# Performance work log

Hardware: AMD Instinct MI355X
Metric: run time of the kernel (lower is better)

## Reference

```python
import jax, jax.numpy as jnp
import numpy as np

DIM = 512
L = 4096
B, H, W = 8, 64, 64
EPS = 1e-06
BN_EPS = 1e-05


def setup_inputs() -> dict:
    key = jax.random.key(0)
    ks = jax.random.split(key, 16)
    s = 1.0 / np.sqrt(DIM)
    d = {
        'x': jax.random.normal(ks[0], (B, DIM, H, W), dtype=jnp.float32),
        'pos_emb': jax.random.normal(ks[1], (1, L, DIM), dtype=jnp.float32),
        'Wq': jax.random.uniform(ks[2], (DIM, DIM), jnp.float32, -s, s),
        'bq': jax.random.uniform(ks[3], (DIM,), jnp.float32, -s, s),
        'Wk': jax.random.uniform(ks[4], (DIM, DIM), jnp.float32, -s, s),
        'bk': jax.random.uniform(ks[5], (DIM,), jnp.float32, -s, s),
        'Wv': jax.random.uniform(ks[6], (DIM, DIM), jnp.float32, -s, s),
        'bv': jax.random.uniform(ks[7], (DIM,), jnp.float32, -s, s),
        'Wq1': jax.random.uniform(ks[8], (DIM, DIM), jnp.float32, -s, s),
        'bq1': jax.random.uniform(ks[9], (DIM,), jnp.float32, -s, s),
        'Wk1': jax.random.uniform(ks[10], (DIM, DIM), jnp.float32, -s, s),
        'bk1': jax.random.uniform(ks[11], (DIM,), jnp.float32, -s, s),
        'gamma': jax.random.normal(ks[12], (1,), jnp.float32) * 0.1,
        'bn_weight': jnp.ones((DIM,), jnp.float32),
        'bn_bias': jnp.zeros((DIM,), jnp.float32),
    }
    return d


def reference(x, pos_emb, Wq, bq, Wk, bk, Wv, bv, Wq1, bq1, Wk1, bk1, gamma, bn_weight, bn_bias):
    Bb, C, Hh, Ww = x.shape
    # [B,C,H,W] -> [B, L, C] tokens
    xs = x.transpose(0, 2, 3, 1).reshape(Bb, Hh * Ww, C) + pos_emb
    Q = jax.nn.relu(xs @ Wq.T + bq)   # kernel_fun = ReLU
    K = jax.nn.relu(xs @ Wk.T + bk)
    V = xs @ Wv.T + bv
    Q1 = xs @ Wq1.T + bq1
    K1 = xs @ Wk1.T + bk1
    # torch einsum 'blc,bcc,bl->blc' uses only diag(KV); compute it directly:
    # diagKV[b,c] = sum_l K[b,l,c] * V[b,l,c]
    diagKV = jnp.einsum('blc,blc->bc', K, V)
    Ksum = K.sum(axis=1)  # == K^T summed over last axis, [B,C]
    Z = 1.0 / jnp.einsum('blc,bc->bl', Q, Ksum + EPS)
    result = Q * diagKV[:, None, :] * Z[:, :, None]  # [B,L,C]
    # channel-softmax attention: softmax over last dim of Q1^T @ K1, [B,C,C]
    mid = jax.nn.softmax(jnp.einsum('blc,bld->bcd', Q1, K1), axis=-1)
    result = result @ mid  # [B,L,C]
    xs = xs + gamma * result
    y = xs.transpose(0, 2, 1).reshape(Bb, C, Hh, Ww)
    # BatchNorm2d in training mode (fresh module): batch stats, biased variance
    mean = y.mean(axis=(0, 2, 3))
    var = y.var(axis=(0, 2, 3))
    yn = (y - mean[None, :, None, None]) * jax.lax.rsqrt(var + BN_EPS)[None, :, None, None]
    yn = yn * bn_weight[None, :, None, None] + bn_bias[None, :, None, None]
    return jax.nn.relu(yn)
```

## Files before the change

kernel.cpp:

```cpp
#include <hip/hip_runtime.h>
#include <stdint.h>

typedef float f32x4 __attribute__((ext_vector_type(4)));
typedef short bf16x8 __attribute__((ext_vector_type(8)));

__device__ __forceinline__ float bf2f(unsigned short h){
  union { unsigned int u; float f; } v; v.u = ((unsigned int)h) << 16; return v.f;
}
__device__ __forceinline__ unsigned short f2bf(float f){
  union { float f; unsigned int u; } v; v.f = f;
  return (unsigned short)((v.u + 0x7fffu + ((v.u >> 16) & 1u)) >> 16);
}

typedef __attribute__((address_space(1))) const unsigned int ga_u32;
typedef __attribute__((address_space(3))) unsigned int ls_u32;
__device__ __forceinline__ void async_load16(const void* g, void* l){
  __builtin_amdgcn_global_load_lds((ga_u32*)g, (ls_u32*)l, 16, 0, 0);
}

#define CFENCE() asm volatile("" ::: "memory")
#define SB0() __builtin_amdgcn_sched_barrier(0)

__global__ __launch_bounds__(256) void k_prep_w(
    const float* __restrict__ w0, const float* __restrict__ w1,
    const float* __restrict__ w2, const float* __restrict__ w3,
    const float* __restrict__ w4, unsigned short* __restrict__ out)
{
  int i = blockIdx.x * 256 + threadIdx.x;
  const float* w = (blockIdx.y == 0) ? w0 : (blockIdx.y == 1) ? w1 :
                   (blockIdx.y == 2) ? w2 : (blockIdx.y == 3) ? w3 : w4;
  out[(size_t)blockIdx.y * 262144 + i] = f2bf(w[i]);
}
__global__ __launch_bounds__(256) void k_prep_b(
    const float* __restrict__ b0, const float* __restrict__ b1,
    const float* __restrict__ b2, const float* __restrict__ b3,
    const float* __restrict__ b4, float* __restrict__ out)
{
  int i = blockIdx.x * 256 + threadIdx.x;
  int s = i >> 9, r = i & 511;
  const float* b = (s == 0) ? b0 : (s == 1) ? b1 : (s == 2) ? b2 : (s == 3) ? b3 : b4;
  out[i] = b[r];
}
__global__ __launch_bounds__(256) void k_prep_dup(
    const unsigned short* __restrict__ wbf, unsigned short* __restrict__ wq1x2)
{
  const int e = blockIdx.x;
  const int t = threadIdx.x;
  #pragma unroll
  for (int rep = 0; rep < 2; rep++){
    int idx = rep*256 + t;
    unsigned short v = wbf[3*262144 + e*512 + idx];
    wq1x2[(size_t)e*1024 + idx] = v;
    wq1x2[(size_t)e*1024 + 512 + idx] = v;
  }
}

__global__ __launch_bounds__(256) void k_build_xs(
    const float* __restrict__ x, const float* __restrict__ pos,
    unsigned short* __restrict__ xsb, unsigned short* __restrict__ xsT,
    float* __restrict__ svec)
{
  __shared__ float tile[64][65];
  __shared__ unsigned short tile2[64][72];
  __shared__ float sred[256];
  const int lt = blockIdx.x, ct = blockIdx.y;
  const int t = threadIdx.x;
  const int rr = t >> 3, c8 = (t & 7) * 8;
  float pr[16];
  #pragma unroll
  for (int pass = 0; pass < 2; pass++){
    int gl = lt*64 + rr + pass*32;
    f32x4 p0 = *(const f32x4*)(pos + (size_t)gl * 512 + ct*64 + c8);
    f32x4 p1 = *(const f32x4*)(pos + (size_t)gl * 512 + ct*64 + c8 + 4);
    #pragma unroll
    for (int s = 0; s < 4; s++){ pr[pass*8+s] = p0[s]; pr[pass*8+4+s] = p1[s]; }
  }
  for (int b = 0; b < 8; b++){
    #pragma unroll
    for (int pass = 0; pass < 2; pass++){
      int r = rr + pass * 32;
      const float* src = x + ((size_t)b * 512 + ct*64 + r) * 4096 + lt*64 + c8;
      f32x4 v0 = *(const f32x4*)src;
      f32x4 v1 = *(const f32x4*)(src + 4);
      #pragma unroll
      for (int s = 0; s < 4; s++){ tile[r][c8+s] = v0[s]; tile[r][c8+4+s] = v1[s]; }
    }
    __syncthreads();
    #pragma unroll
    for (int pass = 0; pass < 2; pass++){
      int ll = rr + pass * 32;
      int gl = lt*64 + ll;
      bf16x8 hv;
      #pragma unroll
      for (int s = 0; s < 8; s++){
        unsigned short h = f2bf(tile[c8+s][ll] + pr[pass*8+s]);
        hv[s] = (short)h;
        tile2[c8+s][ll] = h;
      }
      *(bf16x8*)(xsb + ((size_t)b * 4096 + gl) * 512 + ct*64 + c8) = hv;
    }
    __syncthreads();
    #pragma unroll
    for (int rep = 0; rep < 2; rep++){
      int c = rep*32 + (t >> 3);
      int l0 = (t & 7) * 8;
      bf16x8 v = *(const bf16x8*)&tile2[c][l0];
      *(bf16x8*)(xsT + ((size_t)b * 512 + ct*64 + c) * 4096 + lt*64 + l0) = v;
    }
    {
      const int c = t & 63, lq = t >> 6;
      float s_ = 0.f;
      #pragma unroll
      for (int j = 0; j < 16; j++) s_ += bf2f(tile2[c][lq*16 + j]);
      sred[t] = s_;
      __syncthreads();
      if (t < 64){
        float ss = sred[t] + sred[t+64] + sred[t+128] + sred[t+192];
        atomicAdd(&svec[b*512 + ct*64 + t], ss);
      }
    }
    __syncthreads();
  }
}

__global__ __launch_bounds__(256) void k_uw(
    const unsigned short* __restrict__ wbf, const float* __restrict__ svec,
    float* __restrict__ u, float* __restrict__ w)
{
  __shared__ float sv[512];
  const int sel = blockIdx.x, b = blockIdx.y;
  const int t = threadIdx.x;
  sv[t] = svec[b*512 + t]; sv[t+256] = svec[b*512 + t + 256];
  __syncthreads();
  const unsigned short* Wp = wbf + (size_t)(3 + sel) * 262144;
  float* o = sel ? w : u;
  #pragma unroll
  for (int rep = 0; rep < 2; rep++){
    int e = rep*256 + t;
    const unsigned short* row = Wp + (size_t)e * 512;
    float acc = 0.f;
    for (int ch = 0; ch < 64; ch++){
      bf16x8 v = *(const bf16x8*)(row + ch*8);
      #pragma unroll
      for (int j = 0; j < 8; j++) acc += bf2f((unsigned short)v[j]) * sv[ch*8+j];
    }
    o[b*512 + e] = acc;
  }
}

__global__ __launch_bounds__(256) void k_z(
    const unsigned short* __restrict__ Qb, const float* __restrict__ ksum,
    float* __restrict__ Z)
{
  const int row = blockIdx.x * 4 + (threadIdx.x >> 6);
  const int lane = threadIdx.x & 63;
  const int b = row >> 12;
  bf16x8 q = *(const bf16x8*)(Qb + (size_t)row * 512 + lane * 8);
  f32x4 k0 = *(const f32x4*)(ksum + b*512 + lane*8);
  f32x4 k1 = *(const f32x4*)(ksum + b*512 + lane*8 + 4);
  float den = 0.f;
  #pragma unroll
  for (int s = 0; s < 4; s++) den += bf2f((unsigned short)q[s])   * (k0[s] + 1e-6f);
  #pragma unroll
  for (int s = 0; s < 4; s++) den += bf2f((unsigned short)q[4+s]) * (k1[s] + 1e-6f);
  #pragma unroll
  for (int m = 1; m < 64; m <<= 1) den += __shfl_xor(den, m);
  if (lane == 0) Z[row] = 1.0f / den;
}

__global__ __launch_bounds__(64) void k_softmax(
    const float* __restrict__ S, unsigned short* __restrict__ mid)
{
  const size_t row = blockIdx.x;
  const int lane = threadIdx.x;
  const float* p = S + row * 512 + lane * 8;
  f32x4 v0 = *(const f32x4*)p, v1 = *(const f32x4*)(p + 4);
  float mx = v0[0];
  #pragma unroll
  for (int s = 1; s < 4; s++) mx = fmaxf(mx, v0[s]);
  #pragma unroll
  for (int s = 0; s < 4; s++) mx = fmaxf(mx, v1[s]);
  #pragma unroll
  for (int m = 1; m < 64; m <<= 1) mx = fmaxf(mx, __shfl_xor(mx, m));
  float e[8]; float sum = 0.f;
  #pragma unroll
  for (int s = 0; s < 4; s++){ e[s]   = __expf(v0[s] - mx); sum += e[s]; }
  #pragma unroll
  for (int s = 0; s < 4; s++){ e[4+s] = __expf(v1[s] - mx); sum += e[4+s]; }
  #pragma unroll
  for (int m = 1; m < 64; m <<= 1) sum += __shfl_xor(sum, m);
  float inv = 1.0f / sum;
  bf16x8 hv;
  #pragma unroll
  for (int s = 0; s < 8; s++) hv[s] = (short)f2bf(e[s] * inv);
  *(bf16x8*)(mid + row * 512 + lane * 8) = hv;
}

__global__ __launch_bounds__(256) void k_transpose_scale(
    const unsigned short* __restrict__ in, const float* __restrict__ diag,
    unsigned short* __restrict__ out)
{
  __shared__ float tile[64][65];
  const int rt = blockIdx.x, ct = blockIdx.y, z = blockIdx.z;
  const unsigned short* src = in  + (size_t)z * 262144;
  unsigned short*       dst = out + (size_t)z * 262144;
  const int t = threadIdx.x;
  const int rr = t >> 3, c8 = (t & 7) * 8;
  #pragma unroll
  for (int pass = 0; pass < 2; pass++){
    int r = rr + pass * 32;
    bf16x8 v = *(const bf16x8*)(src + (size_t)(rt*64 + r) * 512 + ct*64 + c8);
    #pragma unroll
    for (int s = 0; s < 8; s++) tile[r][c8+s] = bf2f((unsigned short)v[s]);
  }
  __syncthreads();
  f32x4 dg0 = *(const f32x4*)(diag + z*512 + rt*64 + c8);
  f32x4 dg1 = *(const f32x4*)(diag + z*512 + rt*64 + c8 + 4);
  #pragma unroll
  for (int pass = 0; pass < 2; pass++){
    int c = rr + pass * 32;
    bf16x8 hv;
    #pragma unroll
    for (int s = 0; s < 4; s++) hv[s]   = (short)f2bf(tile[c8+s][c]   * dg0[s]);
    #pragma unroll
    for (int s = 0; s < 4; s++) hv[4+s] = (short)f2bf(tile[c8+4+s][c] * dg1[s]);
    *(bf16x8*)(dst + (size_t)(ct*64 + c) * 512 + rt*64 + c8) = hv;
  }
}

#define GEMM_PRE()                                                            \
  const int tid = threadIdx.x;                                                \
  const int lane = tid & 63;                                                  \
  const int wave = tid >> 6;                                                  \
  const int wm = wave >> 1, wn = wave & 1;                                    \
  size_t aoff[4], boff[4]; int ldsq[4];                                       \
  _Pragma("unroll")                                                           \
  for (int i = 0; i < 4; i++){                                                \
    int qq = i*4 + wave;                                                      \
    int ch = qq*64 + lane;                                                    \
    int m  = ch >> 3, p = ch & 7;                                             \
    int lc = p ^ (m & 7);                                                     \
    aoff[i] = (size_t)(m0 + m) * K + lc*8;                                    \
    boff[i] = (size_t)m * K + lc*8;                                           \
    ldsq[i] = qq * 1024;                                                      \
  }                                                                           \
  f32x4 acc[4][4];                                                            \
  const f32x4 vzero = {0.f,0.f,0.f,0.f};                                      \
  _Pragma("unroll")                                                           \
  for (int i = 0; i < 4; i++)                                                 \
    _Pragma("unroll")                                                         \
    for (int j = 0; j < 4; j++) acc[i][j] = vzero;                            \
  int arow[4], brow[4];                                                       \
  _Pragma("unroll")                                                           \
  for (int f = 0; f < 4; f++){                                                \
    arow[f] = (wm*64 + f*16 + (lane & 15)) * 64;                              \
    brow[f] = (wn*64 + f*16 + (lane & 15)) * 64;                              \
  }                                                                           \
  const int kg = lane >> 4;                                                   \
  const int l7 = lane & 7;                                                    \
  const int l15 = lane & 15;

#define GEMM_STAGE2(buf, kt, BB)                                              \
  _Pragma("unroll")                                                           \
  for (int i = 0; i < 4; i++){                                                \
    async_load16(Ae + aoff[i] + (kt)*64, (char*)&smem[(buf)*8192] + ldsq[i]); \
    async_load16((BB) + boff[i] + (kt)*64, (char*)&smem[16384 + (buf)*8192] + ldsq[i]); \
  }

#define GEMM_COMPUTE2(buf, ACC)                                               \
  _Pragma("unroll")                                                           \
  for (int ks = 0; ks < 2; ks++){                                             \
    bf16x8 a[4], b[4];                                                        \
    const int pa = (ks*4 + kg) ^ l7;                                          \
    _Pragma("unroll")                                                         \
    for (int f = 0; f < 4; f++){                                              \
      a[f] = *(const bf16x8*)&smem[(buf)*8192 + arow[f] + pa*8];              \
      b[f] = *(const bf16x8*)&smem[16384 + (buf)*8192 + brow[f] + pa*8];      \
    }                                                                         \
    _Pragma("unroll")                                                         \
    for (int i = 0; i < 4; i++)                                               \
      _Pragma("unroll")                                                       \
      for (int j = 0; j < 4; j++)                                             \
        (ACC)[i][j] = __builtin_amdgcn_mfma_f32_16x16x32_bf16(a[i], b[j], (ACC)[i][j], 0, 0, 0); \
  }

#define GEMM_KLOOP2(nkt, BB)                                                  \
  GEMM_STAGE2(0, 0, BB);                                                      \
  __syncthreads();                                                            \
  { int cur = 0;                                                              \
    for (int kt = 0; kt < (nkt); kt++){                                       \
      if (kt + 1 < (nkt)) { GEMM_STAGE2(cur ^ 1, kt + 1, BB); }               \
      GEMM_COMPUTE2(cur, acc);                                                \
      __syncthreads();                                                        \
      cur ^= 1;                                                               \
    } }

__global__ __launch_bounds__(256) void gemm_G(
    const unsigned short* __restrict__ A,
    unsigned short* __restrict__ Gstk)
{
  __shared__ unsigned short smem[32768];
  const int bid = blockIdx.x;
  const int wgid = (bid & 7) * 32 + (bid >> 3);
  const int part = wgid & 1;
  const int ntile = (wgid >> 1) & 3;
  const int mtile = (wgid >> 3) & 3;
  const int z = wgid >> 5;
  const int m0 = mtile * 128, n0 = ntile * 128;
  const int K = 4096;
  const unsigned short* Ae = A + (size_t)z * 2097152 + part * 2048;
  const unsigned short* Be = Ae + (size_t)n0 * 4096;

  GEMM_PRE();
  GEMM_KLOOP2(32, Be);

  #pragma unroll
  for (int j = 0; j < 4; j++){
    const int cl = wn*64 + j*16 + l15;
    #pragma unroll
    for (int i = 0; i < 4; i++){
      const int rb = wm*64 + i*16 + kg*4;
      #pragma unroll
      for (int q = 0; q < 4; q++)
        smem[(rb + q)*136 + cl] = f2bf(acc[i][j][q]);
    }
  }
  __syncthreads();
  #pragma unroll
  for (int rep = 0; rep < 8; rep++){
    const int rl = rep*16 + (tid >> 4);
    const int c0 = (tid & 15) * 8;
    bf16x8 v = *(const bf16x8*)&smem[rl*136 + c0];
    *(bf16x8*)(Gstk + (size_t)z*524288 + (size_t)(m0 + rl)*1024 + part*512 + n0 + c0) = v;
  }
}

__global__ __launch_bounds__(256) void gemm_P(
    const unsigned short* __restrict__ Wq1x2,
    const unsigned short* __restrict__ Gstk,
    unsigned short* __restrict__ P)
{
  __shared__ unsigned short smem[32768];
  const int bid = blockIdx.x;
  const int wgid = (bid & 7) * 16 + (bid >> 3);
  const int z = wgid >> 4;
  const int mtile = (wgid >> 2) & 3, ntile = wgid & 3;
  const int m0 = mtile * 128, n0 = ntile * 128;
  const int K = 1024;
  const unsigned short* Ae = Wq1x2;
  const unsigned short* Be = Gstk + (size_t)z * 524288 + (size_t)n0 * 1024;

  GEMM_PRE();
  GEMM_KLOOP2(16, Be);

  #pragma unroll
  for (int j = 0; j < 4; j++){
    const int cl = wn*64 + j*16 + l15;
    #pragma unroll
    for (int i = 0; i < 4; i++){
      const int rb = wm*64 + i*16 + kg*4;
      #pragma unroll
      for (int q = 0; q < 4; q++)
        smem[(rb + q)*136 + cl] = f2bf(acc[i][j][q]);
    }
  }
  __syncthreads();
  #pragma unroll
  for (int rep = 0; rep < 8; rep++){
    const int rl = rep*16 + (tid >> 4);
    const int c0 = (tid & 15) * 8;
    bf16x8 v = *(const bf16x8*)&smem[rl*136 + c0];
    *(bf16x8*)(P + (size_t)z * 262144 + (size_t)(m0 + rl) * 512 + n0 + c0) = v;
  }
}

__global__ __launch_bounds__(256) void gemm_S(
    const unsigned short* __restrict__ P,
    const unsigned short* __restrict__ Wk1b,
    const float* __restrict__ bias5,
    const float* __restrict__ u, const float* __restrict__ w,
    float* __restrict__ Sf)
{
  __shared__ unsigned short smem[32768];
  const int bid = blockIdx.x;
  const int wgid = (bid & 7) * 16 + (bid >> 3);
  const int z = wgid >> 4;
  const int mtile = (wgid >> 2) & 3, ntile = wgid & 3;
  const int m0 = mtile * 128, n0 = ntile * 128;
  const int K = 512;
  const unsigned short* Ae = P + (size_t)z * 262144;
  const unsigned short* Be = Wk1b + (size_t)n0 * 512;

  GEMM_PRE();
  GEMM_KLOOP2(8, Be);

  #pragma unroll
  for (int j = 0; j < 4; j++){
    int cd = n0 + wn*64 + j*16 + l15;
    float bkv = bias5[2048 + cd];
    float wv  = w[z*512 + cd] + 4096.0f * bkv;
    #pragma unroll
    for (int i = 0; i < 4; i++){
      int r = m0 + wm*64 + i*16 + kg*4;
      #pragma unroll
      for (int q = 0; q < 4; q++){
        int rr = r + q;
        float uq  = u[z*512 + rr];
        float bqv = bias5[1536 + rr];
        Sf[(size_t)z * 262144 + (size_t)rr * 512 + cd] =
            acc[i][j][q] + uq * bkv + bqv * wv;
      }
    }
  }
}

__global__ __launch_bounds__(256, 2) void gemm_proj2(
    const unsigned short* __restrict__ A,
    const unsigned short* __restrict__ W,
    const float* __restrict__ bias5,
    unsigned short* __restrict__ Qb,
    float* __restrict__ diag, float* __restrict__ ksum)
{
  __shared__ unsigned short smem[32768];
  const int bid = blockIdx.x;
  const int wgid = (bid & 7) * 256 + (bid >> 3);
  const int mtile = wgid >> 3;
  const int unit  = wgid & 7;
  const int m0 = mtile * 128;
  const int K = 512;
  const unsigned short* Ae = A;

  int mode, cb;
  const unsigned short* BeK; const unsigned short* BeV = W;
  if (unit < 4){ mode = 0; cb = unit*128;     BeK = W + (size_t)cb * 512; }
  else         { mode = 1; cb = (unit-4)*128; BeK = W + 262144 + (size_t)cb * 512;
                                              BeV = W + 524288 + (size_t)cb * 512; }

  GEMM_PRE();

  if (mode == 1){
    const int bz = mtile >> 5;
    GEMM_STAGE2(0, 0, BeK);
    __syncthreads();
    int cur = 0;
    for (int kt = 0; kt < 8; kt++){
      if (kt < 7) { GEMM_STAGE2(cur ^ 1, kt + 1, BeK); }
      else        { GEMM_STAGE2(cur ^ 1, 0, BeV); }
      GEMM_COMPUTE2(cur, acc);
      __syncthreads();
      cur ^= 1;
    }
    GEMM_STAGE2(cur ^ 1, 1, BeV);
    unsigned int kpk[4][4][2];
    #pragma unroll
    for (int j = 0; j < 4; j++){
      const int cj = cb + wn*64 + j*16 + l15;
      const float bb = bias5[512 + cj];
      float ks_ = 0.f;
      #pragma unroll
      for (int i = 0; i < 4; i++){
        #pragma unroll
        for (int h = 0; h < 2; h++){
          float v0 = acc[i][j][2*h]   + bb; v0 = v0 > 0.f ? v0 : 0.f;
          float v1 = acc[i][j][2*h+1] + bb; v1 = v1 > 0.f ? v1 : 0.f;
          unsigned short h0 = f2bf(v0), h1 = f2bf(v1);
          kpk[i][j][h] = (unsigned)h0 | ((unsigned)h1 << 16);
          ks_ += bf2f(h0) + bf2f(h1);
        }
        acc[i][j] = vzero;
      }
      ks_ += __shfl_xor(ks_, 16);
      ks_ += __shfl_xor(ks_, 32);
      if (lane < 16) atomicAdd(&ksum[bz*512 + cj], ks_);
    }
    for (int kt = 0; kt < 8; kt++){
      if (kt >= 1 && kt < 7) { GEMM_STAGE2(cur ^ 1, kt + 1, BeV); }
      GEMM_COMPUTE2(cur, acc);
      __syncthreads();
      cur ^= 1;
    }
    #pragma unroll
    for (int j = 0; j < 4; j++){
      const int cj = cb + wn*64 + j*16 + l15;
      const float bb = bias5[1024 + cj];
      float dv = 0.f;
      #pragma unroll
      for (int i = 0; i < 4; i++){
        #pragma unroll
        for (int h = 0; h < 2; h++){
          float v0 = bf2f(f2bf(acc[i][j][2*h]   + bb));
          float v1 = bf2f(f2bf(acc[i][j][2*h+1] + bb));
          dv += bf2f((unsigned short)(kpk[i][j][h] & 0xffffu)) * v0
              + bf2f((unsigned short)(kpk[i][j][h] >> 16))     * v1;
        }
      }
      dv += __shfl_xor(dv, 16);
      dv += __shfl_xor(dv, 32);
      if (lane < 16) atomicAdd(&diag[bz*512 + cj], dv);
    }
    return;
  }

  GEMM_KLOOP2(8, BeK);

  #pragma unroll
  for (int j = 0; j < 4; j++){
    const int cl = wn*64 + j*16 + l15;
    const float bb = bias5[cb + cl];
    #pragma unroll
    for (int i = 0; i < 4; i++){
      const int rb = wm*64 + i*16 + kg*4;
      #pragma unroll
      for (int q = 0; q < 4; q++){
        float v = acc[i][j][q] + bb; v = v > 0.f ? v : 0.f;
        smem[(rb + q)*136 + cl] = f2bf(v);
      }
    }
  }
  __syncthreads();
  #pragma unroll
  for (int rep = 0; rep < 8; rep++){
    const int rl = rep*16 + (tid >> 4);
    const int c0 = (tid & 15) * 8;
    bf16x8 v = *(const bf16x8*)&smem[rl*136 + c0];
    *(bf16x8*)(Qb + (size_t)(m0 + rl) * 512 + cb + c0) = v;
  }
}

#define G8_PRE(AE)                                                            \
  const int t = threadIdx.x;                                                  \
  const int lane = t & 63;                                                    \
  const int wave = t >> 6;                                                    \
  const int wm = wave >> 2, wn = wave & 3;                                    \
  const int l15 = lane & 15, kg = lane >> 4;                                  \
  const int lcw = ((t & 7) ^ ((t >> 3) & 7)) * 8;                             \
  const unsigned short* a_src = (AE) + (size_t)(m0 + (t >> 3)) * 512 + lcw;   \
  f32x4 acc[8][4];                                                            \
  const f32x4 vzero = {0.f,0.f,0.f,0.f};                                      \
  _Pragma("unroll")                                                           \
  for (int i = 0; i < 8; i++)                                                 \
    _Pragma("unroll")                                                         \
    for (int j = 0; j < 4; j++) acc[i][j] = vzero;                            \
  bf16x8 af[4][2], bf[4][2];

#define STAGE_A(D,H,TT) do{                                                   \
  async_load16(a_src + (H)*65536 + (TT)*64,                                   \
               (char*)smem + ((D)*16384 + (H)*8192 + t*8)*2);                 \
  async_load16(a_src + (H)*65536 + 32768 + (TT)*64,                           \
               (char*)smem + ((D)*16384 + (H)*8192 + 4096 + t*8)*2);          \
}while(0)

#define STAGE_B(D,H,TT) do{                                                   \
  async_load16(b_src + (H)*65536 + (TT)*64,                                   \
               (char*)smem + (32768 + (D)*16384 + (H)*8192 + t*8)*2);         \
  async_load16(b_src + (H)*65536 + 32768 + (TT)*64,                           \
               (char*)smem + (32768 + (D)*16384 + (H)*8192 + 4096 + t*8)*2);  \
}while(0)

#define READ_A(D, MH) do{                                                     \
  _Pragma("unroll")                                                           \
  for (int mfl = 0; mfl < 4; ++mfl){                                          \
    const int rl = ((MH)*4 + mfl)*16 + l15;                                   \
    _Pragma("unroll")                                                         \
    for (int ks = 0; ks < 2; ++ks){                                           \
      const int ck = (ks*4 + kg) ^ (rl & 7);                                  \
      af[mfl][ks] = *(const bf16x8*)&smem[(D)*16384 + wm*8192 + rl*64 + ck*8];\
    }                                                                         \
  }                                                                           \
}while(0)

#define READ_B(D, NP) do{                                                     \
  _Pragma("unroll")                                                           \
  for (int nfl = 0; nfl < 2; ++nfl){                                          \
    const int nf = (NP)*2 + nfl;                                              \
    const int rbl = (wn & 1)*64 + nf*16 + l15;                                \
    _Pragma("unroll")                                                         \
    for (int ks = 0; ks < 2; ++ks){                                           \
      const int ck = (ks*4 + kg) ^ (rbl & 7);                                 \
      bf[nf][ks] = *(const bf16x8*)&smem[32768 + (D)*16384 + (wn>>1)*8192 + rbl*64 + ck*8]; \
    }                                                                         \
  }                                                                           \
}while(0)

#define QUAD(MH, NP)                                                          \
  _Pragma("unroll")                                                           \
  for (int mfl = 0; mfl < 4; ++mfl)                                           \
    _Pragma("unroll")                                                         \
    for (int nfl = 0; nfl < 2; ++nfl)                                         \
      _Pragma("unroll")                                                       \
      for (int ks = 0; ks < 2; ++ks)                                          \
        acc[(MH)*4+mfl][(NP)*2+nfl] = __builtin_amdgcn_mfma_f32_16x16x32_bf16(\
            af[mfl][ks], bf[(NP)*2+nfl][ks], acc[(MH)*4+mfl][(NP)*2+nfl], 0,0,0);

#define PH_MID()  CFENCE(); __builtin_amdgcn_s_barrier();                     \
  __builtin_amdgcn_s_setprio(1); SB0()
#define PH_END()  SB0(); __builtin_amdgcn_s_setprio(0); CFENCE();             \
  __builtin_amdgcn_s_barrier(); CFENCE()
#define PH_END_VM4() SB0(); __builtin_amdgcn_s_setprio(0);                    \
  asm volatile("s_waitcnt vmcnt(4)" ::: "memory");                            \
  __builtin_amdgcn_s_barrier(); CFENCE()
#define PH_END_VM0() SB0(); __builtin_amdgcn_s_setprio(0);                    \
  asm volatile("s_waitcnt vmcnt(0)" ::: "memory");                            \
  __builtin_amdgcn_s_barrier(); CFENCE()

#define G8_KLOOP()                                                            \
  STAGE_A(0,0,0); STAGE_A(0,1,0); STAGE_B(0,0,0); STAGE_B(0,1,0);             \
  STAGE_B(1,0,1); STAGE_B(1,1,1);                                             \
  asm volatile("s_waitcnt vmcnt(4)" ::: "memory");                            \
  __builtin_amdgcn_s_barrier(); CFENCE();                                     \
  for (int it = 0; it < 3; ++it){                                             \
    const int t1 = 2*it + 1, t2 = 2*it + 2, t3 = 2*it + 3;                    \
    READ_A(0,0); READ_B(0,0); STAGE_A(1,0,t1);                                \
    PH_MID(); QUAD(0,0); PH_END();                                            \
    READ_B(0,1); STAGE_A(1,1,t1);                                             \
    PH_MID(); QUAD(0,1); PH_END();                                            \
    READ_A(0,1); STAGE_B(0,0,t2);                                             \
    PH_MID(); QUAD(1,0); PH_END();                                            \
    STAGE_A(0,0,t2);                                                          \
    PH_MID(); QUAD(1,1); PH_END_VM4();                                        \
    READ_A(1,0); READ_B(1,0); STAGE_A(0,1,t2);                                \
    PH_MID(); QUAD(0,0); PH_END();                                            \
    READ_B(1,1); STAGE_B(0,1,t2);                                             \
    PH_MID(); QUAD(0,1); PH_END();                                            \
    READ_A(1,1); STAGE_B(1,0,t3);                                             \
    PH_MID(); QUAD(1,0); PH_END();                                            \
    STAGE_B(1,1,t3);                                                          \
    PH_MID(); QUAD(1,1); PH_END_VM4();                                        \
  }                                                                           \
  { READ_A(0,0); READ_B(0,0); STAGE_A(1,0,7);                                 \
    PH_MID(); QUAD(0,0); PH_END();                                            \
    READ_B(0,1); STAGE_A(1,1,7);                                              \
    PH_MID(); QUAD(0,1); PH_END();                                            \
    READ_A(0,1);                                                              \
    PH_MID(); QUAD(1,0); PH_END();                                            \
    PH_MID(); QUAD(1,1); PH_END_VM0();                                        \
    READ_A(1,0); READ_B(1,0);                                                 \
    PH_MID(); QUAD(0,0); PH_END();                                            \
    READ_B(1,1);                                                              \
    PH_MID(); QUAD(0,1); PH_END();                                            \
    READ_A(1,1);                                                              \
    PH_MID(); QUAD(1,0); PH_END();                                            \
    PH_MID(); QUAD(1,1); PH_END(); }

__global__ __launch_bounds__(512, 2) void gemm8_res(
    const unsigned short* __restrict__ A,
    const unsigned short* __restrict__ Bt,
    const float* __restrict__ Zp,
    unsigned short* __restrict__ outh,
    const float* __restrict__ gamma_p,
    float* __restrict__ bnS, float* __restrict__ bnQ)
{
  __shared__ unsigned short smem[65536];
  __shared__ float zbuf[256];
  const int bid = blockIdx.x;
  const int wgid = (bid & 7) * 32 + (bid >> 3);
  const int mtile = wgid >> 1;
  const int ntile = wgid & 1;
  const int m0 = mtile * 256;
  const int nc0 = ntile * 256;

  G8_PRE(A);
  const unsigned short* b_src =
      Bt + (size_t)(mtile >> 4) * 262144 + (size_t)(nc0 + (t >> 3)) * 512 + lcw;

  G8_KLOOP();

  const float g = gamma_p[0];
  __syncthreads();
  if (t < 256) zbuf[t] = Zp[m0 + t];
  __syncthreads();
  #pragma unroll
  for (int nf = 0; nf < 4; nf++){
    int cl = wn*64 + nf*16 + l15;
    #pragma unroll
    for (int mf = 0; mf < 8; mf++){
      int rbase = wm*128 + mf*16 + kg*4;
      #pragma unroll
      for (int q = 0; q < 4; q++){
        int rl = rbase + q;
        smem[rl*256 + (cl ^ (((rl >> 2) & 3) << 4))] =
            f2bf(g * zbuf[rl] * acc[mf][nf][q]);
      }
    }
  }
  __syncthreads();
  float sc[8] = {0.f,0.f,0.f,0.f,0.f,0.f,0.f,0.f};
  float sq[8] = {0.f,0.f,0.f,0.f,0.f,0.f,0.f,0.f};
  const int c0 = (t & 31) * 8;
  #pragma unroll
  for (int rep = 0; rep < 16; rep++){
    int rl = rep*16 + (t >> 5);
    bf16x8 ga = *(const bf16x8*)&smem[rl*256 + (c0 ^ (((rl >> 2) & 3) << 4))];
    size_t gidx = (size_t)(m0 + rl) * 512 + nc0 + c0;
    bf16x8 xv = *(const bf16x8*)(outh + gidx);
    bf16x8 yv;
    #pragma unroll
    for (int j = 0; j < 8; j++){
      float y = bf2f((unsigned short)xv[j]) + bf2f((unsigned short)ga[j]);
      yv[j] = (short)f2bf(y);
      sc[j] += y; sq[j] += y * y;
    }
    *(bf16x8*)(outh + gidx) = yv;
  }
  __syncthreads();
  float* red = (float*)(void*)smem;
  const int tg = t >> 5;
  f32x4 s0 = {sc[0],sc[1],sc[2],sc[3]}, s1 = {sc[4],sc[5],sc[6],sc[7]};
  f32x4 q0 = {sq[0],sq[1],sq[2],sq[3]}, q1 = {sq[4],sq[5],sq[6],sq[7]};
  *(f32x4*)&red[tg*256 + c0]        = s0;  *(f32x4*)&red[tg*256 + c0 + 4]        = s1;
  *(f32x4*)&red[4096 + tg*256 + c0] = q0;  *(f32x4*)&red[4096 + tg*256 + c0 + 4] = q1;
  __syncthreads();
  if (t < 256){
    float ss = 0.f, qq = 0.f;
    #pragma unroll
    for (int gg = 0; gg < 16; gg++){
      ss += red[gg*256 + t];
      qq += red[4096 + gg*256 + t];
    }
    atomicAdd(&bnS[nc0 + t], ss);
    atomicAdd(&bnQ[nc0 + t], qq);
  }
}

__global__ __launch_bounds__(256) void k_bn_finalize(
    const unsigned short* __restrict__ y, const float* __restrict__ bnS,
    const float* __restrict__ bnQ, const float* __restrict__ bnw,
    const float* __restrict__ bnb, float* __restrict__ out)
{
  __shared__ float tile[64][65];
  __shared__ float scale_s[64], shift_s[64];
  const int lt = blockIdx.x, ct = blockIdx.y, b = blockIdx.z;
  const int t = threadIdx.x;
  if (t < 64){
    int c = ct*64 + t;
    float s = bnS[c], q = bnQ[c];
    float mean = s * (1.0f / 32768.0f);
    float var  = q * (1.0f / 32768.0f) - mean * mean;
    float inv  = rsqrtf(var + 1e-5f);
    float scv  = bnw[c] * inv;
    scale_s[t] = scv;
    shift_s[t] = bnb[c] - mean * scv;
  }
  const int rr = t >> 3, c8 = (t & 7) * 8;
  #pragma unroll
  for (int pass = 0; pass < 2; pass++){
    int l = rr + pass * 32;
    bf16x8 v = *(const bf16x8*)(y + ((size_t)b * 4096 + lt*64 + l) * 512 + ct*64 + c8);
    #pragma unroll
    for (int s = 0; s < 8; s++) tile[l][c8+s] = bf2f((unsigned short)v[s]);
  }
  __syncthreads();
  #pragma unroll
  for (int pass = 0; pass < 2; pass++){
    int c = rr + pass * 32;
    float scv = scale_s[c], sh = shift_s[c];
    f32x4 o0, o1;
    #pragma unroll
    for (int s = 0; s < 4; s++){
      float v = tile[c8+s][c] * scv + sh;     o0[s] = v > 0.f ? v : 0.f;
      float w = tile[c8+4+s][c] * scv + sh;   o1[s] = w > 0.f ? w : 0.f;
    }
    float* dp = out + ((size_t)b * 512 + ct*64 + c) * 4096 + lt*64 + c8;
    *(f32x4*)dp = o0;
    *(f32x4*)(dp + 4) = o1;
  }
}

extern "C" void kernel_launch(void* const* d_in, const int* in_sizes, int n_in,
                              void* d_out, int out_size, void* d_ws, size_t ws_size,
                              hipStream_t stream)
{
  const float* x    = (const float*)d_in[0];
  const float* pos  = (const float*)d_in[1];
  const float* Wq   = (const float*)d_in[2];
  const float* bq   = (const float*)d_in[3];
  const float* Wk   = (const float*)d_in[4];
  const float* bk   = (const float*)d_in[5];
  const float* Wv   = (const float*)d_in[6];
  const float* bv   = (const float*)d_in[7];
  const float* Wq1  = (const float*)d_in[8];
  const float* bq1  = (const float*)d_in[9];
  const float* Wk1  = (const float*)d_in[10];
  const float* bk1  = (const float*)d_in[11];
  const float* gam  = (const float*)d_in[12];
  const float* bnw  = (const float*)d_in[13];
  const float* bnb  = (const float*)d_in[14];
  float* out = (float*)d_out;
  char* ws = (char*)d_ws;

  const size_t MB = 1ull << 20;
  const size_t OFF_XSB  = 0;
  const size_t OFF_QB   = 32*MB;
  const size_t OFF_XST  = 64*MB;
  const size_t OFF_GSTK = 96*MB;
  const size_t OFF_PBF  = 104*MB;
  const size_t OFF_SF   = 108*MB;
  const size_t OFF_MIDB = 116*MB;
  const size_t OFF_MIDT = 120*MB;
  const size_t OFF_WBF  = 124*MB;
  const size_t OFF_WQ2  = 127*MB;
  const size_t OFF_B5   = 128*MB + 512*1024;
  const size_t OFF_UV   = 129*MB;
  const size_t OFF_WV   = OFF_UV + 16384;
  const size_t OFF_Z    = OFF_WV + 16384;
  const size_t OFF_DIAG = 130*MB;
  const size_t OFF_KSUM = OFF_DIAG + 16384;
  const size_t OFF_BNS  = OFF_KSUM + 16384;
  const size_t OFF_BNQ  = OFF_BNS + 2048;
  const size_t OFF_SV   = OFF_BNQ + 2048;
  const size_t ZERO_LEN = 16384 + 16384 + 2048 + 2048 + 16384;
  const size_t WS_NEED  = OFF_SV + 16384;
  if (ws_size < WS_NEED) return;

  unsigned short* xsb  = (unsigned short*)(ws + OFF_XSB);
  unsigned short* Qb   = (unsigned short*)(ws + OFF_QB);
  unsigned short* xsT  = (unsigned short*)(ws + OFF_XST);
  unsigned short* Gstk = (unsigned short*)(ws + OFF_GSTK);
  unsigned short* Pbf  = (unsigned short*)(ws + OFF_PBF);
  float*          Sf   = (float*)(ws + OFF_SF);
  unsigned short* midb = (unsigned short*)(ws + OFF_MIDB);
  unsigned short* midT = (unsigned short*)(ws + OFF_MIDT);
  unsigned short* wbf  = (unsigned short*)(ws + OFF_WBF);
  unsigned short* wq1x2= (unsigned short*)(ws + OFF_WQ2);
  float* bias5 = (float*)(ws + OFF_B5);
  float* uvec = (float*)(ws + OFF_UV);
  float* wvec = (float*)(ws + OFF_WV);
  float* Zp   = (float*)(ws + OFF_Z);
  float* diag = (float*)(ws + OFF_DIAG);
  float* ksum = (float*)(ws + OFF_KSUM);
  float* bnS  = (float*)(ws + OFF_BNS);
  float* bnQ  = (float*)(ws + OFF_BNQ);
  float* svec = (float*)(ws + OFF_SV);

  hipMemsetAsync(ws + OFF_DIAG, 0, ZERO_LEN, stream);

  k_prep_w  <<<dim3(1024, 5), 256, 0, stream>>>(Wq, Wk, Wv, Wq1, Wk1, wbf);
  k_prep_b  <<<dim3(10),      256, 0, stream>>>(bq, bk, bv, bq1, bk1, bias5);
  k_prep_dup<<<dim3(512),     256, 0, stream>>>(wbf, wq1x2);

  k_build_xs<<<dim3(64, 8), 256, 0, stream>>>(x, pos, xsb, xsT, svec);

  gemm_proj2<<<dim3(2048), 256, 0, stream>>>(xsb, wbf, bias5, Qb, diag, ksum);

  k_uw<<<dim3(2, 8), 256, 0, stream>>>(wbf, svec, uvec, wvec);

  gemm_G<<<dim3(256), 256, 0, stream>>>(xsT, Gstk);

  gemm_P<<<dim3(128), 256, 0, stream>>>(wq1x2, Gstk, Pbf);
  gemm_S<<<dim3(128), 256, 0, stream>>>(Pbf, wbf + 4*262144, bias5, uvec, wvec, Sf);

  k_z<<<dim3(8192), 256, 0, stream>>>(Qb, ksum, Zp);

  k_softmax<<<dim3(4096), 64, 0, stream>>>(Sf, midb);
  k_transpose_scale<<<dim3(8, 8, 8), 256, 0, stream>>>(midb, diag, midT);

  gemm8_res<<<dim3(256), 512, 0, stream>>>(Qb, midT, Zp, xsb, gam, bnS, bnQ);

  k_bn_finalize<<<dim3(64, 8, 8), 256, 0, stream>>>(xsb, bnS, bnQ, bnw, bnb, out);
}
```

Measured before the change: 246.1 us.

## Merge prep kernels and co-schedule Gram, projection and u/w work in one launch

The three weight/bias prep kernels are folded into a single launch, and the Wq1 duplicate is now converted straight from fp32 so it no longer depends on the earlier bf16 copy. The Gram GEMM (gemm_G), the projection GEMM (gemm_proj2) and the small u/w matvec (k_uw) are combined into one mega-kernel that dispatches on block index, with the long K=4096 Gram tiles placed first. The aim is to cut launch gaps and let the long Gram blocks overlap with the many short projection tiles instead of running serially. In exchange the Gram path is now limited by the launch_bounds(256,2) occupancy hint of the merged kernel, and k_z is moved ahead of gemm_P/S.

```diff
diff --git a/kernel.cpp b/kernel.cpp
--- a/kernel.cpp
+++ b/kernel.cpp
@@ -21,37 +21,39 @@
 #define CFENCE() asm volatile("" ::: "memory")
 #define SB0() __builtin_amdgcn_sched_barrier(0)
 
-__global__ __launch_bounds__(256) void k_prep_w(
+__global__ __launch_bounds__(256) void k_prep_all(
     const float* __restrict__ w0, const float* __restrict__ w1,
     const float* __restrict__ w2, const float* __restrict__ w3,
-    const float* __restrict__ w4, unsigned short* __restrict__ out)
-{
-  int i = blockIdx.x * 256 + threadIdx.x;
-  const float* w = (blockIdx.y == 0) ? w0 : (blockIdx.y == 1) ? w1 :
-                   (blockIdx.y == 2) ? w2 : (blockIdx.y == 3) ? w3 : w4;
-  out[(size_t)blockIdx.y * 262144 + i] = f2bf(w[i]);
-}
-__global__ __launch_bounds__(256) void k_prep_b(
+    const float* __restrict__ w4,
     const float* __restrict__ b0, const float* __restrict__ b1,
     const float* __restrict__ b2, const float* __restrict__ b3,
-    const float* __restrict__ b4, float* __restrict__ out)
-{
-  int i = blockIdx.x * 256 + threadIdx.x;
-  int s = i >> 9, r = i & 511;
-  const float* b = (s == 0) ? b0 : (s == 1) ? b1 : (s == 2) ? b2 : (s == 3) ? b3 : b4;
-  out[i] = b[r];
-}
-__global__ __launch_bounds__(256) void k_prep_dup(
-    const unsigned short* __restrict__ wbf, unsigned short* __restrict__ wq1x2)
-{
-  const int e = blockIdx.x;
+    const float* __restrict__ b4,
+    unsigned short* __restrict__ wbf, float* __restrict__ bias5,
+    unsigned short* __restrict__ wq1x2)
+{
+  const int bid = blockIdx.x;
   const int t = threadIdx.x;
-  #pragma unroll
-  for (int rep = 0; rep < 2; rep++){
-    int idx = rep*256 + t;
-    unsigned short v = wbf[3*262144 + e*512 + idx];
-    wq1x2[(size_t)e*1024 + idx] = v;
-    wq1x2[(size_t)e*1024 + 512 + idx] = v;
+  if (bid < 5120){
+    int slot = bid >> 10;
+    int i = (bid & 1023) * 256 + t;
+    const float* w = (slot == 0) ? w0 : (slot == 1) ? w1 :
+                     (slot == 2) ? w2 : (slot == 3) ? w3 : w4;
+    wbf[(size_t)slot * 262144 + i] = f2bf(w[i]);
+  } else if (bid < 5130){
+    int i = (bid - 5120) * 256 + t;
+    int s = i >> 9, r = i & 511;
+    const float* b = (s == 0) ? b0 : (s == 1) ? b1 : (s == 2) ? b2 :
+                     (s == 3) ? b3 : b4;
+    bias5[i] = b[r];
+  } else {
+    int e = bid - 5130;
+    #pragma unroll
+    for (int rep = 0; rep < 2; rep++){
+      int idx = rep*256 + t;
+      unsigned short v = f2bf(w3[e*512 + idx]);
+      wq1x2[(size_t)e*1024 + idx] = v;
+      wq1x2[(size_t)e*1024 + 512 + idx] = v;
+    }
   }
 }
 
@@ -120,31 +122,6 @@
       }
     }
     __syncthreads();
-  }
-}
-
-__global__ __launch_bounds__(256) void k_uw(
-    const unsigned short* __restrict__ wbf, const float* __restrict__ svec,
-    float* __restrict__ u, float* __restrict__ w)
-{
-  __shared__ float sv[512];
-  const int sel = blockIdx.x, b = blockIdx.y;
-  const int t = threadIdx.x;
-  sv[t] = svec[b*512 + t]; sv[t+256] = svec[b*512 + t + 256];
-  __syncthreads();
-  const unsigned short* Wp = wbf + (size_t)(3 + sel) * 262144;
-  float* o = sel ? w : u;
-  #pragma unroll
-  for (int rep = 0; rep < 2; rep++){
-    int e = rep*256 + t;
-    const unsigned short* row = Wp + (size_t)e * 512;
-    float acc = 0.f;
-    for (int ch = 0; ch < 64; ch++){
-      bf16x8 v = *(const bf16x8*)(row + ch*8);
-      #pragma unroll
-      for (int j = 0; j < 8; j++) acc += bf2f((unsigned short)v[j]) * sv[ch*8+j];
-    }
-    o[b*512 + e] = acc;
   }
 }
 
@@ -295,137 +272,84 @@
       cur ^= 1;                                                               \
     } }
 
-__global__ __launch_bounds__(256) void gemm_G(
+__global__ __launch_bounds__(256, 2) void k_mega(
     const unsigned short* __restrict__ A,
-    unsigned short* __restrict__ Gstk)
+    const unsigned short* __restrict__ xsT,
+    const unsigned short* __restrict__ W,
+    const float* __restrict__ bias5,
+    const float* __restrict__ svec,
+    unsigned short* __restrict__ Qb,
+    unsigned short* __restrict__ Gstk,
+    float* __restrict__ diag, float* __restrict__ ksum,
+    float* __restrict__ uvec, float* __restrict__ wvec)
 {
   __shared__ unsigned short smem[32768];
   const int bid = blockIdx.x;
-  const int wgid = (bid & 7) * 32 + (bid >> 3);
-  const int part = wgid & 1;
-  const int ntile = (wgid >> 1) & 3;
-  const int mtile = (wgid >> 3) & 3;
-  const int z = wgid >> 5;
-  const int m0 = mtile * 128, n0 = ntile * 128;
-  const int K = 4096;
-  const unsigned short* Ae = A + (size_t)z * 2097152 + part * 2048;
-  const unsigned short* Be = Ae + (size_t)n0 * 4096;
-
-  GEMM_PRE();
-  GEMM_KLOOP2(32, Be);
-
-  #pragma unroll
-  for (int j = 0; j < 4; j++){
-    const int cl = wn*64 + j*16 + l15;
-    #pragma unroll
-    for (int i = 0; i < 4; i++){
-      const int rb = wm*64 + i*16 + kg*4;
-      #pragma unroll
-      for (int q = 0; q < 4; q++)
-        smem[(rb + q)*136 + cl] = f2bf(acc[i][j][q]);
-    }
-  }
-  __syncthreads();
-  #pragma unroll
-  for (int rep = 0; rep < 8; rep++){
-    const int rl = rep*16 + (tid >> 4);
-    const int c0 = (tid & 15) * 8;
-    bf16x8 v = *(const bf16x8*)&smem[rl*136 + c0];
-    *(bf16x8*)(Gstk + (size_t)z*524288 + (size_t)(m0 + rl)*1024 + part*512 + n0 + c0) = v;
-  }
-}
-
-__global__ __launch_bounds__(256) void gemm_P(
-    const unsigned short* __restrict__ Wq1x2,
-    const unsigned short* __restrict__ Gstk,
-    unsigned short* __restrict__ P)
-{
-  __shared__ unsigned short smem[32768];
-  const int bid = blockIdx.x;
-  const int wgid = (bid & 7) * 16 + (bid >> 3);
-  const int z = wgid >> 4;
-  const int mtile = (wgid >> 2) & 3, ntile = wgid & 3;
-  const int m0 = mtile * 128, n0 = ntile * 128;
-  const int K = 1024;
-  const unsigned short* Ae = Wq1x2;
-  const unsigned short* Be = Gstk + (size_t)z * 524288 + (size_t)n0 * 1024;
-
-  GEMM_PRE();
-  GEMM_KLOOP2(16, Be);
-
-  #pragma unroll
-  for (int j = 0; j < 4; j++){
-    const int cl = wn*64 + j*16 + l15;
-    #pragma unroll
-    for (int i = 0; i < 4; i++){
-      const int rb = wm*64 + i*16 + kg*4;
-      #pragma unroll
-      for (int q = 0; q < 4; q++)
-        smem[(rb + q)*136 + cl] = f2bf(acc[i][j][q]);
-    }
-  }
-  __syncthreads();
-  #pragma unroll
-  for (int rep = 0; rep < 8; rep++){
-    const int rl = rep*16 + (tid >> 4);
-    const int c0 = (tid & 15) * 8;
-    bf16x8 v = *(const bf16x8*)&smem[rl*136 + c0];
-    *(bf16x8*)(P + (size_t)z * 262144 + (size_t)(m0 + rl) * 512 + n0 + c0) = v;
-  }
-}
-
-__global__ __launch_bounds__(256) void gemm_S(
-    const unsigned short* __restrict__ P,
-    const unsigned short* __restrict__ Wk1b,
-    const float* __restrict__ bias5,
-    const float* __restrict__ u, const float* __restrict__ w,
-    float* __restrict__ Sf)
-{
-  __shared__ unsigned short smem[32768];
-  const int bid = blockIdx.x;
-  const int wgid = (bid & 7) * 16 + (bid >> 3);
-  const int z = wgid >> 4;
-  const int mtile = (wgid >> 2) & 3, ntile = wgid & 3;
-  const int m0 = mtile * 128, n0 = ntile * 128;
-  const int K = 512;
-  const unsigned short* Ae = P + (size_t)z * 262144;
-  const unsigned short* Be = Wk1b + (size_t)n0 * 512;
-
-  GEMM_PRE();
-  GEMM_KLOOP2(8, Be);
-
-  #pragma unroll
-  for (int j = 0; j < 4; j++){
-    int cd = n0 + wn*64 + j*16 + l15;
-    float bkv = bias5[2048 + cd];
-    float wv  = w[z*512 + cd] + 4096.0f * bkv;
-    #pragma unroll
-    for (int i = 0; i < 4; i++){
-      int r = m0 + wm*64 + i*16 + kg*4;
-      #pragma unroll
-      for (int q = 0; q < 4; q++){
-        int rr = r + q;
-        float uq  = u[z*512 + rr];
-        float bqv = bias5[1536 + rr];
-        Sf[(size_t)z * 262144 + (size_t)rr * 512 + cd] =
-            acc[i][j][q] + uq * bkv + bqv * wv;
+  const int xcd = bid & 7, local = bid >> 3;
+
+  if (local < 32){
+    const int gw = xcd*32 + local;
+    const int part = gw & 1;
+    const int ntile = (gw >> 1) & 3;
+    const int mtile = (gw >> 3) & 3;
+    const int z = gw >> 5;
+    const int m0 = mtile * 128, n0 = ntile * 128;
+    const int K = 4096;
+    const unsigned short* Ae = xsT + (size_t)z * 2097152 + part * 2048;
+    const unsigned short* Be = Ae + (size_t)n0 * 4096;
+
+    GEMM_PRE();
+    GEMM_KLOOP2(32, Be);
+
+    #pragma unroll
+    for (int j = 0; j < 4; j++){
+      const int cl = wn*64 + j*16 + l15;
+      #pragma unroll
+      for (int i = 0; i < 4; i++){
+        const int rb = wm*64 + i*16 + kg*4;
+        #pragma unroll
+        for (int q = 0; q < 4; q++)
+          smem[(rb + q)*136 + cl] = f2bf(acc[i][j][q]);
       }
     }
-  }
-}
-
-__global__ __launch_bounds__(256, 2) void gemm_proj2(
-    const unsigned short* __restrict__ A,
-    const unsigned short* __restrict__ W,
-    const float* __restrict__ bias5,
-    unsigned short* __restrict__ Qb,
-    float* __restrict__ diag, float* __restrict__ ksum)
-{
-  __shared__ unsigned short smem[32768];
-  const int bid = blockIdx.x;
-  const int wgid = (bid & 7) * 256 + (bid >> 3);
-  const int mtile = wgid >> 3;
-  const int unit  = wgid & 7;
+    __syncthreads();
+    #pragma unroll
+    for (int rep = 0; rep < 8; rep++){
+      const int rl = rep*16 + (tid >> 4);
+      const int c0 = (tid & 15) * 8;
+      bf16x8 v = *(const bf16x8*)&smem[rl*136 + c0];
+      *(bf16x8*)(Gstk + (size_t)z*524288 + (size_t)(m0 + rl)*1024 + part*512 + n0 + c0) = v;
+    }
+    return;
+  }
+
+  if (local >= 288){
+    const int uwid = xcd*2 + (local - 288);
+    const int sel = uwid & 1, b = uwid >> 1;
+    const int t = threadIdx.x;
+    float* sv = (float*)(void*)smem;
+    sv[t] = svec[b*512 + t]; sv[t+256] = svec[b*512 + t + 256];
+    __syncthreads();
+    const unsigned short* Wp = W + (size_t)(3 + sel) * 262144;
+    float* o = sel ? wvec : uvec;
+    #pragma unroll
+    for (int rep = 0; rep < 2; rep++){
+      int e = rep*256 + t;
+      const unsigned short* row = Wp + (size_t)e * 512;
+      float acc_ = 0.f;
+      for (int ch = 0; ch < 64; ch++){
+        bf16x8 v = *(const bf16x8*)(row + ch*8);
+        #pragma unroll
+        for (int j = 0; j < 8; j++) acc_ += bf2f((unsigned short)v[j]) * sv[ch*8+j];
+      }
+      o[b*512 + e] = acc_;
+    }
+    return;
+  }
+
+  const int pw = xcd*256 + (local - 32);
+  const int mtile = pw >> 3;
+  const int unit  = pw & 7;
   const int m0 = mtile * 128;
   const int K = 512;
   const unsigned short* Ae = A;
@@ -524,6 +448,85 @@
     const int c0 = (tid & 15) * 8;
     bf16x8 v = *(const bf16x8*)&smem[rl*136 + c0];
     *(bf16x8*)(Qb + (size_t)(m0 + rl) * 512 + cb + c0) = v;
+  }
+}
+
+__global__ __launch_bounds__(256) void gemm_P(
+    const unsigned short* __restrict__ Wq1x2,
+    const unsigned short* __restrict__ Gstk,
+    unsigned short* __restrict__ P)
+{
+  __shared__ unsigned short smem[32768];
+  const int bid = blockIdx.x;
+  const int wgid = (bid & 7) * 16 + (bid >> 3);
+  const int z = wgid >> 4;
+  const int mtile = (wgid >> 2) & 3, ntile = wgid & 3;
+  const int m0 = mtile * 128, n0 = ntile * 128;
+  const int K = 1024;
+  const unsigned short* Ae = Wq1x2;
+  const unsigned short* Be = Gstk + (size_t)z * 524288 + (size_t)n0 * 1024;
+
+  GEMM_PRE();
+  GEMM_KLOOP2(16, Be);
+
+  #pragma unroll
+  for (int j = 0; j < 4; j++){
+    const int cl = wn*64 + j*16 + l15;
+    #pragma unroll
+    for (int i = 0; i < 4; i++){
+      const int rb = wm*64 + i*16 + kg*4;
+      #pragma unroll
+      for (int q = 0; q < 4; q++)
+        smem[(rb + q)*136 + cl] = f2bf(acc[i][j][q]);
+    }
+  }
+  __syncthreads();
+  #pragma unroll
+  for (int rep = 0; rep < 8; rep++){
+    const int rl = rep*16 + (tid >> 4);
+    const int c0 = (tid & 15) * 8;
+    bf16x8 v = *(const bf16x8*)&smem[rl*136 + c0];
+    *(bf16x8*)(P + (size_t)z * 262144 + (size_t)(m0 + rl) * 512 + n0 + c0) = v;
+  }
+}
+
+__global__ __launch_bounds__(256) void gemm_S(
+    const unsigned short* __restrict__ P,
+    const unsigned short* __restrict__ Wk1b,
+    const float* __restrict__ bias5,
+    const float* __restrict__ u, const float* __restrict__ w,
+    float* __restrict__ Sf)
+{
+  __shared__ unsigned short smem[32768];
+  const int bid = blockIdx.x;
+  const int wgid = (bid & 7) * 16 + (bid >> 3);
+  const int z = wgid >> 4;
+  const int mtile = (wgid >> 2) & 3, ntile = wgid & 3;
+  const int m0 = mtile * 128, n0 = ntile * 128;
+  const int K = 512;
+  const unsigned short* Ae = P + (size_t)z * 262144;
+  const unsigned short* Be = Wk1b + (size_t)n0 * 512;
+
+  GEMM_PRE();
+  GEMM_KLOOP2(8, Be);
+
+  #pragma unroll
+  for (int j = 0; j < 4; j++){
+    int cd = n0 + wn*64 + j*16 + l15;
+    float bkv = bias5[2048 + cd];
+    float wv  = w[z*512 + cd] + 4096.0f * bkv;
+    #pragma unroll
+    for (int i = 0; i < 4; i++){
+      int r = m0 + wm*64 + i*16 + kg*4;
+      #pragma unroll
+      for (int q = 0; q < 4; q++){
+        int rr = r + q;
+        float uq  = u[z*512 + rr];
+        float bqv = bias5[1536 + rr];
+        Sf[(size_t)z * 262144 + (size_t)rr * 512 + cd] =
+            acc[i][j][q] + uq * bkv + bqv * wv;
+      }
+    }
   }
 }
 
@@ -834,23 +837,20 @@
 
   hipMemsetAsync(ws + OFF_DIAG, 0, ZERO_LEN, stream);
 
-  k_prep_w  <<<dim3(1024, 5), 256, 0, stream>>>(Wq, Wk, Wv, Wq1, Wk1, wbf);
-  k_prep_b  <<<dim3(10),      256, 0, stream>>>(bq, bk, bv, bq1, bk1, bias5);
-  k_prep_dup<<<dim3(512),     256, 0, stream>>>(wbf, wq1x2);
+  k_prep_all<<<dim3(5642), 256, 0, stream>>>(Wq, Wk, Wv, Wq1, Wk1,
+                                             bq, bk, bv, bq1, bk1,
+                                             wbf, bias5, wq1x2);
 
   k_build_xs<<<dim3(64, 8), 256, 0, stream>>>(x, pos, xsb, xsT, svec);
 
-  gemm_proj2<<<dim3(2048), 256, 0, stream>>>(xsb, wbf, bias5, Qb, diag, ksum);
-
-  k_uw<<<dim3(2, 8), 256, 0, stream>>>(wbf, svec, uvec, wvec);
-
-  gemm_G<<<dim3(256), 256, 0, stream>>>(xsT, Gstk);
+  k_mega<<<dim3(2320), 256, 0, stream>>>(xsb, xsT, wbf, bias5, svec,
+                                         Qb, Gstk, diag, ksum, uvec, wvec);
+
+  k_z<<<dim3(8192), 256, 0, stream>>>(Qb, ksum, Zp);
 
   gemm_P<<<dim3(128), 256, 0, stream>>>(wq1x2, Gstk, Pbf);
   gemm_S<<<dim3(128), 256, 0, stream>>>(Pbf, wbf + 4*262144, bias5, uvec, wvec, Sf);
 
-  k_z<<<dim3(8192), 256, 0, stream>>>(Qb, ksum, Zp);
-
   k_softmax<<<dim3(4096), 64, 0, stream>>>(Sf, midb);
   k_transpose_scale<<<dim3(8, 8, 8), 256, 0, stream>>>(midb, diag, midT);
 
```

After: 219.4 us. -10.8%, faster.
